# Kernel optimization log

Measured on AMD Instinct MI355X. Metric: run time of the kernel, lower is better.

The kernel has to match this reference:

```python
import jax, jax.numpy as jnp
import numpy as np

DT = 0.04
CUBIC = 0.008
NUM_STEPS = 30
EPS_LN = 1e-5  # torch LayerNorm default eps


def _signals(embed_w, ids):
    # embedding lookup -> LayerNorm (no affine, biased var) -> L2 normalize
    emb = embed_w[ids]  # [..., D]
    mu = emb.mean(-1, keepdims=True)
    var = emb.var(-1, keepdims=True)
    emb = (emb - mu) / jnp.sqrt(var + EPS_LN)
    n = jnp.maximum(jnp.linalg.norm(emb, axis=-1, keepdims=True), 1e-12)
    return emb / n


def _step(s, diffusion, sig):
    # state drift: GEMM + cubic nonlinearity around the per-row mean
    c = s - s.mean(-1, keepdims=True)
    drift = s @ diffusion.T + CUBIC * c ** 3 + sig
    s2 = s + DT * drift
    s2 = jnp.nan_to_num(s2, nan=0.0, posinf=0.0, neginf=0.0)
    return jnp.clip(s2, -80.0, 80.0)


def _converge(s, diffusion, sig):
    def body(state, _):
        return _step(state, diffusion, sig), None
    s, _ = jax.lax.scan(body, s, None, length=NUM_STEPS)
    return s


def setup_inputs() -> dict:
    key = jax.random.key(0)
    k1, k2, k3 = jax.random.split(key, 3)
    B, T, V, D = 256, 32, 50257, 512
    input_ids = jax.random.randint(k1, (B, T), 0, V)
    embed_w = jax.random.normal(k2, (V, D), jnp.float32)
    diffusion = jax.random.normal(k3, (D, D), jnp.float32) * 0.02  # mildly contractive like make_diffusion_matrix
    temperature_raw = jnp.array([np.log(np.exp(0.12) - 1.0)], jnp.float32)  # softplus^-1(0.12)
    return {"input_ids": input_ids, "embed_w": embed_w,
            "diffusion": diffusion, "temperature_raw": temperature_raw}


def reference(input_ids, embed_w, diffusion, temperature_raw):
    B, T = input_ids.shape
    V, D = embed_w.shape
    sigs = _signals(embed_w, input_ids)  # [B, T, D]

    def tok_body(state, sig_t):  # sig_t: [B, D]
        return _converge(state, diffusion, sig_t), None

    state0 = jnp.zeros((B, D), embed_w.dtype)
    state, _ = jax.lax.scan(tok_body, state0, jnp.swapaxes(sigs, 0, 1))  # [B, D]

    # next_token_logits: -cdist(state, all_signals) / softplus(temp)
    all_sigs = _signals(embed_w, jnp.arange(V))  # [V, D]
    sq = (jnp.sum(state ** 2, -1, keepdims=True)
          + jnp.sum(all_sigs ** 2, -1)[None, :]
          - 2.0 * state @ all_sigs.T)
    dists = jnp.sqrt(jnp.maximum(sq, 0.0))  # [B, V]
    temp = jnp.maximum(jax.nn.softplus(temperature_raw[0]), 1e-6)
    logits = -dists / temp
    logits = jnp.nan_to_num(logits, nan=0.0, posinf=0.0, neginf=-10000.0)
    return logits
```

## Files before the change

### kernel.cpp

```cpp
#include <hip/hip_runtime.h>


static constexpr int   kB     = 256;
static constexpr int   kT     = 32;
static constexpr int   kV     = 50257;
static constexpr int   kD     = 512;
static constexpr int   kSteps = 30;
static constexpr float kDT    = 0.04f;
static constexpr float kCubic = 0.008f;
static constexpr float kEpsLN = 1e-5f;

static constexpr int RR          = 3;
static constexpr int SCAN_BLOCKS = (kB + RR - 1) / RR;
static constexpr int VT          = 32;

__global__ __launch_bounds__(128)
void k_signals(const float* __restrict__ emb, float* __restrict__ sigs) {
  const int row = blockIdx.x;
  const int tid = threadIdx.x;
  const float4 x = reinterpret_cast<const float4*>(emb + (size_t)row * kD)[tid];
  float s = x.x + x.y + x.z + x.w;
  float q = x.x * x.x + x.y * x.y + x.z * x.z + x.w * x.w;
#pragma unroll
  for (int o = 32; o > 0; o >>= 1) {
    s += __shfl_xor(s, o);
    q += __shfl_xor(q, o);
  }
  __shared__ float ls[2], lq[2];
  const int wid = tid >> 6;
  if ((tid & 63) == 0) { ls[wid] = s; lq[wid] = q; }
  __syncthreads();
  s = ls[0] + ls[1];
  q = lq[0] + lq[1];
  const float mu   = s * (1.0f / kD);
  const float var  = fmaxf(q * (1.0f / kD) - mu * mu, 0.0f);
  const float rstd = rsqrtf(var + kEpsLN);
  const float n     = rstd * sqrtf((float)kD * var);
  const float scale = rstd / fmaxf(n, 1e-12f);
  float4 y;
  y.x = (x.x - mu) * scale;
  y.y = (x.y - mu) * scale;
  y.z = (x.z - mu) * scale;
  y.w = (x.w - mu) * scale;
  reinterpret_cast<float4*>(sigs + (size_t)row * kD)[tid] = y;
}

__global__ __launch_bounds__(256)
void k_wprep(const float* __restrict__ dif, float4* __restrict__ w4) {
  const int idx = blockIdx.x * 256 + threadIdx.x;
  const int c = idx >> 9;
  const int j = idx & 511;
  w4[idx] = reinterpret_cast<const float4*>(dif + (size_t)j * kD)[c];
}

__global__ __launch_bounds__(512)
void k_scan(const int* __restrict__ ids, const float* __restrict__ sigs,
            const float4* __restrict__ w4, float* __restrict__ state,
            float* __restrict__ ssq) {
  const int tid  = threadIdx.x;
  const int b0   = blockIdx.x * RR;
  const int wid  = tid >> 6;
  const int lane = tid & 63;

  __shared__ float4 s4[RR][kD / 4];
  __shared__ float  red[RR][8];
  float* s_lin = reinterpret_cast<float*>(s4);

  float s_reg[RR], sig[RR];
#pragma unroll
  for (int r = 0; r < RR; ++r) { s_reg[r] = 0.0f; s_lin[r * kD + tid] = 0.0f; }
  __syncthreads();

  for (int t = 0; t < kT; ++t) {
#pragma unroll
    for (int r = 0; r < RR; ++r) {
      int bb = b0 + r; if (bb >= kB) bb = 0;
      const int id = ids[bb * kT + t];
      sig[r] = sigs[(size_t)id * kD + tid];
    }
    for (int step = 0; step < kSteps; ++step) {
      float part[RR];
#pragma unroll
      for (int r = 0; r < RR; ++r) part[r] = s_reg[r];
#pragma unroll
      for (int o = 32; o > 0; o >>= 1) {
#pragma unroll
        for (int r = 0; r < RR; ++r) part[r] += __shfl_xor(part[r], o);
      }
      if (lane == 0) {
#pragma unroll
        for (int r = 0; r < RR; ++r) red[r][wid] = part[r];
      }
      __syncthreads();
      float mean[RR];
#pragma unroll
      for (int r = 0; r < RR; ++r) {
        float m = 0.0f;
#pragma unroll
        for (int w = 0; w < 8; ++w) m += red[r][w];
        mean[r] = m * (1.0f / kD);
      }
      float acc[RR];
#pragma unroll
      for (int r = 0; r < RR; ++r) acc[r] = 0.0f;
      const float4* __restrict__ wp = w4 + tid;
#pragma unroll 4
      for (int c = 0; c < kD / 4; ++c) {
        const float4 w = wp[(size_t)c << 9];
#pragma unroll
        for (int r = 0; r < RR; ++r) {
          const float4 sv = s4[r][c];
          acc[r] = fmaf(sv.x, w.x, acc[r]);
          acc[r] = fmaf(sv.y, w.y, acc[r]);
          acc[r] = fmaf(sv.z, w.z, acc[r]);
          acc[r] = fmaf(sv.w, w.w, acc[r]);
        }
      }
      __syncthreads();
#pragma unroll
      for (int r = 0; r < RR; ++r) {
        const float cc    = s_reg[r] - mean[r];
        const float drift = acc[r] + kCubic * cc * cc * cc + sig[r];
        float sn = fmaf(kDT, drift, s_reg[r]);
        sn = fminf(fmaxf(sn, -80.0f), 80.0f);
        s_reg[r] = sn;
        s_lin[r * kD + tid] = sn;
      }
    }
  }

  {
    float part[RR];
#pragma unroll
    for (int r = 0; r < RR; ++r) part[r] = s_reg[r] * s_reg[r];
#pragma unroll
    for (int o = 32; o > 0; o >>= 1) {
#pragma unroll
      for (int r = 0; r < RR; ++r) part[r] += __shfl_xor(part[r], o);
    }
    if (lane == 0) {
#pragma unroll
      for (int r = 0; r < RR; ++r) red[r][wid] = part[r];
    }
    __syncthreads();
#pragma unroll
    for (int r = 0; r < RR; ++r) {
      const int bb = b0 + r;
      if (bb < kB) {
        state[(size_t)bb * kD + tid] = s_reg[r];
        if (tid == 0) {
          float m = 0.0f;
#pragma unroll
          for (int w = 0; w < 8; ++w) m += red[r][w];
          ssq[bb] = m;
        }
      }
    }
  }
}

__global__ __launch_bounds__(256)
void k_logits(const float* __restrict__ state, const float* __restrict__ ssq,
              const float* __restrict__ sigs, const float* __restrict__ traw,
              float* __restrict__ out) {
  const int tid = threadIdx.x;
  const int v0  = blockIdx.x * VT;
  __shared__ float st[kB][36];
  __shared__ float at[VT][36];
  __shared__ float ssq_l[kB];

  ssq_l[tid] = ssq[tid];

  const int tv = tid & 31;
  const int tb = tid >> 5;
  float acc[32];
#pragma unroll
  for (int i = 0; i < 32; ++i) acc[i] = 0.0f;
  float asq = 0.0f;

  for (int kc = 0; kc < kD / 32; ++kc) {
    __syncthreads();
#pragma unroll
    for (int i = 0; i < 8; ++i) {
      const int flat = tid + 256 * i;
      const int b = flat >> 3, qq = flat & 7;
      const float4 v4 = *reinterpret_cast<const float4*>(
          state + ((size_t)b << 9) + (kc << 5) + (qq << 2));
      *reinterpret_cast<float4*>(&st[b][qq << 2]) = v4;
    }
    {
      const int v = tid >> 3, qq = tid & 7;
      float4 a4 = {0.f, 0.f, 0.f, 0.f};
      if (v0 + v < kV)
        a4 = *reinterpret_cast<const float4*>(
            sigs + ((size_t)(v0 + v) << 9) + (kc << 5) + (qq << 2));
      *reinterpret_cast<float4*>(&at[v][qq << 2]) = a4;
    }
    __syncthreads();
#pragma unroll
    for (int kk = 0; kk < 8; ++kk) {
      const float4 a = *reinterpret_cast<const float4*>(&at[tv][kk << 2]);
      asq = fmaf(a.x, a.x, fmaf(a.y, a.y, fmaf(a.z, a.z, fmaf(a.w, a.w, asq))));
#pragma unroll
      for (int ib = 0; ib < 32; ++ib) {
        const float4 sv = *reinterpret_cast<const float4*>(&st[tb + 8 * ib][kk << 2]);
        acc[ib] = fmaf(sv.x, a.x, acc[ib]);
        acc[ib] = fmaf(sv.y, a.y, acc[ib]);
        acc[ib] = fmaf(sv.z, a.z, acc[ib]);
        acc[ib] = fmaf(sv.w, a.w, acc[ib]);
      }
    }
  }

  const float x  = traw[0];
  const float sp = log1pf(expf(x));
  const float rt = 1.0f / fmaxf(sp, 1e-6f);
  const int v = v0 + tv;
  if (v < kV) {
#pragma unroll
    for (int ib = 0; ib < 32; ++ib) {
      const int b = tb + 8 * ib;
      const float sq = ssq_l[b] + asq - 2.0f * acc[ib];
      out[(size_t)b * kV + v] = -sqrtf(fmaxf(sq, 0.0f)) * rt;
    }
  }
}

extern "C" void kernel_launch(void* const* d_in, const int* in_sizes, int n_in,
                              void* d_out, int out_size, void* d_ws, size_t ws_size,
                              hipStream_t stream) {
  const int*   ids  = (const int*)d_in[0];
  const float* emb  = (const float*)d_in[1];
  const float* dif  = (const float*)d_in[2];
  const float* traw = (const float*)d_in[3];
  float* out = (float*)d_out;

  char* ws = (char*)d_ws;
  size_t off = 0;
  float*  all_sigs = (float*)(ws + off);  off += (size_t)kV * kD * sizeof(float);
  float4* w4       = (float4*)(ws + off); off += (size_t)kD * kD * sizeof(float);
  float*  state    = (float*)(ws + off);  off += (size_t)kB * kD * sizeof(float);
  float*  ssq      = (float*)(ws + off);  off += (size_t)kB * sizeof(float);

  hipLaunchKernelGGL(k_signals, dim3(kV), dim3(128), 0, stream, emb, all_sigs);
  hipLaunchKernelGGL(k_wprep, dim3((kD * kD / 4) / 256), dim3(256), 0, stream, dif, w4);
  hipLaunchKernelGGL(k_scan, dim3(SCAN_BLOCKS), dim3(512), 0, stream,
                     ids, all_sigs, w4, state, ssq);
  hipLaunchKernelGGL(k_logits, dim3((kV + VT - 1) / VT), dim3(256), 0, stream,
                     state, ssq, all_sigs, traw, out);
}
```

Measured before the change: 10.53 ms.

## Use fp16 packed dot2 for scan GEMV with double-buffered weight loads

```diff
diff --git a/kernel.cpp b/kernel.cpp
--- a/kernel.cpp
+++ b/kernel.cpp
@@ -13,6 +13,27 @@
 static constexpr int RR          = 3;
 static constexpr int SCAN_BLOCKS = (kB + RR - 1) / RR;
 static constexpr int VT          = 32;
+
+typedef _Float16 half1;
+typedef _Float16 half2v __attribute__((ext_vector_type(2)));
+union HU { unsigned int u; half2v h; half1 s[2]; };
+
+#if defined(__has_builtin)
+#if __has_builtin(__builtin_amdgcn_fdot2)
+#define HAS_FDOT2 1
+#endif
+#endif
+
+__device__ __forceinline__ float dot2acc(unsigned int a, unsigned int b, float c) {
+  HU ua; ua.u = a;
+  HU ub; ub.u = b;
+#ifdef HAS_FDOT2
+  return __builtin_amdgcn_fdot2(ua.h, ub.h, c, false);
+#else
+  c = fmaf((float)ua.s[0], (float)ub.s[0], c);
+  return fmaf((float)ua.s[1], (float)ub.s[1], c);
+#endif
+}
 
 __global__ __launch_bounds__(128)
 void k_signals(const float* __restrict__ emb, float* __restrict__ sigs) {
@@ -46,30 +67,62 @@
 }
 
 __global__ __launch_bounds__(256)
-void k_wprep(const float* __restrict__ dif, float4* __restrict__ w4) {
+void k_wprep(const float* __restrict__ dif, unsigned int* __restrict__ w2) {
   const int idx = blockIdx.x * 256 + threadIdx.x;
-  const int c = idx >> 9;
-  const int j = idx & 511;
-  w4[idx] = reinterpret_cast<const float4*>(dif + (size_t)j * kD)[c];
+  const int q  = idx & 3;
+  const int j  = (idx >> 2) & 511;
+  const int c  = idx >> 11;
+  const int k0 = c * 8 + q * 2;
+  HU u;
+  u.s[0] = (half1)dif[(size_t)j * kD + k0];
+  u.s[1] = (half1)dif[(size_t)j * kD + k0 + 1];
+  w2[idx] = u.u;
+}
+
+__device__ __forceinline__ void loadw(uint4 (&dst)[8], const uint4* __restrict__ wp,
+                                      int c0) {
+#pragma unroll
+  for (int i = 0; i < 8; ++i) dst[i] = wp[(size_t)((c0 * 8 + i) << 9)];
+}
+
+__device__ __forceinline__ void compw(const uint4 (&w)[8],
+                                      const unsigned short (*__restrict__ sh)[kD],
+                                      int c0, float (&acc)[RR]) {
+#pragma unroll
+  for (int i = 0; i < 8; ++i) {
+    const uint4 wv = w[i];
+#pragma unroll
+    for (int r = 0; r < RR; ++r) {
+      const uint4 sv = *reinterpret_cast<const uint4*>(&sh[r][(c0 * 8 + i) * 8]);
+      float a = acc[r];
+      a = dot2acc(sv.x, wv.x, a);
+      a = dot2acc(sv.y, wv.y, a);
+      a = dot2acc(sv.z, wv.z, a);
+      a = dot2acc(sv.w, wv.w, a);
+      acc[r] = a;
+    }
+  }
 }
 
 __global__ __launch_bounds__(512)
 void k_scan(const int* __restrict__ ids, const float* __restrict__ sigs,
-            const float4* __restrict__ w4, float* __restrict__ state,
+            const uint4* __restrict__ w2, float* __restrict__ state,
             float* __restrict__ ssq) {
   const int tid  = threadIdx.x;
   const int b0   = blockIdx.x * RR;
   const int wid  = tid >> 6;
   const int lane = tid & 63;
 
-  __shared__ float4 s4[RR][kD / 4];
-  __shared__ float  red[RR][8];
-  float* s_lin = reinterpret_cast<float*>(s4);
+  __shared__ unsigned short s_h[RR][kD];
+  __shared__ float red[RR][8];
 
   float s_reg[RR], sig[RR];
 #pragma unroll
-  for (int r = 0; r < RR; ++r) { s_reg[r] = 0.0f; s_lin[r * kD + tid] = 0.0f; }
-  __syncthreads();
+  for (int r = 0; r < RR; ++r) { s_reg[r] = 0.0f; s_h[r][tid] = 0; }
+
+  const uint4* __restrict__ wp = w2 + tid;
+  uint4 wA[8], wB[8];
+  loadw(wA, wp, 0);
 
   for (int t = 0; t < kT; ++t) {
 #pragma unroll
@@ -103,18 +156,12 @@
       float acc[RR];
 #pragma unroll
       for (int r = 0; r < RR; ++r) acc[r] = 0.0f;
-      const float4* __restrict__ wp = w4 + tid;
-#pragma unroll 4
-      for (int c = 0; c < kD / 4; ++c) {
-        const float4 w = wp[(size_t)c << 9];
-#pragma unroll
-        for (int r = 0; r < RR; ++r) {
-          const float4 sv = s4[r][c];
-          acc[r] = fmaf(sv.x, w.x, acc[r]);
-          acc[r] = fmaf(sv.y, w.y, acc[r]);
-          acc[r] = fmaf(sv.z, w.z, acc[r]);
-          acc[r] = fmaf(sv.w, w.w, acc[r]);
-        }
+#pragma unroll
+      for (int np = 0; np < 4; ++np) {
+        loadw(wB, wp, np * 2 + 1);
+        compw(wA, s_h, np * 2, acc);
+        loadw(wA, wp, (np * 2 + 2) & 7);
+        compw(wB, s_h, np * 2 + 1, acc);
       }
       __syncthreads();
 #pragma unroll
@@ -124,7 +171,8 @@
         float sn = fmaf(kDT, drift, s_reg[r]);
         sn = fminf(fmaxf(sn, -80.0f), 80.0f);
         s_reg[r] = sn;
-        s_lin[r * kD + tid] = sn;
+        HU u; u.s[0] = (half1)sn;
+        s_h[r][tid] = (unsigned short)(u.u & 0xffffu);
       }
     }
   }
@@ -237,15 +285,15 @@
 
   char* ws = (char*)d_ws;
   size_t off = 0;
-  float*  all_sigs = (float*)(ws + off);  off += (size_t)kV * kD * sizeof(float);
-  float4* w4       = (float4*)(ws + off); off += (size_t)kD * kD * sizeof(float);
-  float*  state    = (float*)(ws + off);  off += (size_t)kB * kD * sizeof(float);
-  float*  ssq      = (float*)(ws + off);  off += (size_t)kB * sizeof(float);
+  float*        all_sigs = (float*)(ws + off);        off += (size_t)kV * kD * sizeof(float);
+  unsigned int* w2       = (unsigned int*)(ws + off); off += (size_t)kD * kD / 2 * sizeof(unsigned int);
+  float*        state    = (float*)(ws + off);        off += (size_t)kB * kD * sizeof(float);
+  float*        ssq      = (float*)(ws + off);        off += (size_t)kB * sizeof(float);
 
   hipLaunchKernelGGL(k_signals, dim3(kV), dim3(128), 0, stream, emb, all_sigs);
-  hipLaunchKernelGGL(k_wprep, dim3((kD * kD / 4) / 256), dim3(256), 0, stream, dif, w4);
+  hipLaunchKernelGGL(k_wprep, dim3(kD * kD / 2 / 256), dim3(256), 0, stream, dif, w2);
   hipLaunchKernelGGL(k_scan, dim3(SCAN_BLOCKS), dim3(512), 0, stream,
-                     ids, all_sigs, w4, state, ssq);
+                     ids, all_sigs, (const uint4*)w2, state, ssq);
   hipLaunchKernelGGL(k_logits, dim3((kV + VT - 1) / VT), dim3(256), 0, stream,
                      state, ssq, all_sigs, traw, out);
 }
```

Result: faster. 9.304 ms (-11.7%).
